# Optimization experiments

Hardware: AMD Instinct MI355X
Metric: run time of the kernel (lower is better)

## Reference

```python
import jax, jax.numpy as jnp
import numpy as np

TEMP_DIM = 36      # V
HIDDEN   = 128     # d
HEADS    = 4
STATIC   = 16
MAX_LEN  = 500
SEQ_T    = 256
BATCH    = 32


def _xavier(k, shape):
    lim = np.sqrt(6.0 / (shape[0] + shape[1]))
    return jax.random.uniform(k, shape, jnp.float32, -lim, lim)


def setup_inputs() -> dict:
    d, V, S, T, B = HIDDEN, TEMP_DIM, STATIC, SEQ_T, BATCH
    key = jax.random.key(0)
    ks = jax.random.split(key, 16)
    return dict(
        Xtemp=jax.random.normal(ks[0], (T, B, V), jnp.float32),
        Xtimes=jax.random.uniform(ks[1], (T, B, 1), jnp.float32) * MAX_LEN,
        Xstatic=jax.random.normal(ks[2], (B, S), jnp.float32),
        mask=jax.random.randint(ks[3], (T, B, V), 0, 2, jnp.int32),
        # MultiHeadAttention params
        Wq=_xavier(ks[4], (d, d)), Wk=_xavier(ks[5], (d, d)), Wv=_xavier(ks[6], (d, d)),
        # grouped Conv1d(V, V*d, 1, groups=V): per-variable scale+bias -> (V,d)
        temp_w=jax.random.normal(ks[7], (V, d), jnp.float32) * 0.5,
        temp_b=jnp.zeros((V, d), jnp.float32),
        # static embedding Linear(S, V*d)
        emb_W=_xavier(ks[8], (S, V * d)), emb_b=jnp.zeros((V * d,), jnp.float32),
        # MLP: Conv1d(V*d,4d,1)+BN+GELU, Conv1d(4d,d,1)+BN+GELU
        mlp_W1=_xavier(ks[9], (4 * d, V * d)), mlp_b1=jnp.zeros((4 * d,), jnp.float32),
        bn1_g=jnp.ones((4 * d,), jnp.float32), bn1_b=jnp.zeros((4 * d,), jnp.float32),
        mlp_W2=_xavier(ks[10], (d, 4 * d)), mlp_b2=jnp.zeros((d,), jnp.float32),
        bn2_g=jnp.ones((d,), jnp.float32), bn2_b=jnp.zeros((d,), jnp.float32),
        ln_g=jnp.ones((d,), jnp.float32), ln_b=jnp.zeros((d,), jnp.float32),
    )


def _batchnorm(x, g, b):
    # train-mode BatchNorm1d over (B, T) for x:(B, C, T), biased variance, eps=1e-5
    mu = x.mean((0, 2), keepdims=True)
    var = x.var((0, 2), keepdims=True)
    return (x - mu) * jax.lax.rsqrt(var + 1e-5) * g[None, :, None] + b[None, :, None]


def reference(Xtemp, Xtimes, Xstatic, mask, Wq, Wk, Wv, temp_w, temp_b,
              emb_W, emb_b, mlp_W1, mlp_b1, bn1_g, bn1_b,
              mlp_W2, mlp_b2, bn2_g, bn2_b, ln_g, ln_b):
    T, B, V = Xtemp.shape
    d = Wq.shape[0]
    h = HEADS
    dk = d // h

    xt = Xtemp.transpose(1, 2, 0)                      # (B,V,T)
    m = mask.astype(jnp.float32).transpose(1, 2, 0)    # (B,V,T)

    # grouped 1x1 conv == per-variable affine lift to d channels
    Htemp = xt[:, :, None, :] * temp_w[None, :, :, None] + temp_b[None, :, :, None]  # (B,V,d,T)
    Htemp = Htemp.transpose(0, 2, 1, 3)                # (B,d,V,T)

    # positional encoding
    timescales = jnp.power(jnp.float32(MAX_LEN), jnp.linspace(0.0, 1.0, d // 2))
    scaled = Xtimes / timescales                       # (T,B,d//2)
    pe = jnp.concatenate([jnp.sin(scaled), jnp.cos(scaled)], axis=-1)  # (T,B,d)
    Hpos = pe.transpose(1, 2, 0)[:, :, None, :]        # (B,d,1,T)

    emb = (Xstatic @ emb_W + emb_b).reshape(B, V, d).transpose(0, 2, 1)[..., None]  # (B,d,V,1)
    H = Htemp + Hpos + emb                             # (B,d,V,T)

    # masked temporal mean per variable
    mk = m[:, None]                                    # (B,1,V,T)
    h2 = (H * mk).sum(-1)                              # (B,d,V)
    lt = mk.sum(-1) + 1.0                              # (B,1,V)
    h4 = (h2 / lt).transpose(0, 2, 1)                  # (B,V,d)

    # multi-head variable-vs-variable scores
    scale = 1.0 / np.sqrt(dk).astype(np.float32)
    q = (h4 @ Wq).reshape(B, V, h, dk) * scale
    k = (h4 @ Wk).reshape(B, V, h, dk) * scale
    A = jnp.einsum('bvhd,buhd->bhvu', q, k)            # (B,h,V,V)
    mean_v = h4 @ Wv                                   # (B,V,d)

    # per-timestep key masking, broadcast softmax over last (key-variable) dim
    key_mask = m.transpose(0, 2, 1)                    # (B,T,V)
    A4 = A[:, :, None, :, :] - 1e6 * (1.0 - key_mask[:, None, :, None, :])  # (B,h,T,V,V)
    S = jax.nn.softmax(A4, axis=-1)                    # (B,h,T,V,V)

    H2 = H.reshape(B, h, dk, V, T)
    v2 = jnp.einsum('bhtvu,bhdut->bhdvt', S, H2)       # (B,h,dk,V,T)
    v3 = v2.reshape(B, d, V, T)
    v4 = v3 + mean_v.transpose(0, 2, 1)[:, :, :, None]
    v5 = v4.reshape(B, d * V, T)

    y1 = jnp.einsum('bct,oc->bot', v5, mlp_W1) + mlp_b1[None, :, None]
    y1 = jax.nn.gelu(_batchnorm(y1, bn1_g, bn1_b), approximate=False)
    y2 = jnp.einsum('bct,oc->bot', y1, mlp_W2) + mlp_b2[None, :, None]
    z = jax.nn.gelu(_batchnorm(y2, bn2_g, bn2_b), approximate=False)   # (B,d,T)

    # residual LayerNorm over channel dim
    zt = z.transpose(0, 2, 1)                          # (B,T,d)
    mu = zt.mean(-1, keepdims=True)
    var = zt.var(-1, keepdims=True)
    zn = (zt - mu) * jax.lax.rsqrt(var + 1e-5) * ln_g + ln_b
    return z + zn.transpose(0, 2, 1)                   # (B,d,T)
```

## Files before the change

### kernel.cpp

```cpp
#include <hip/hip_runtime.h>
#include <hip/hip_bf16.h>
#include <math.h>

#define T_  256
#define B_  32
#define V_  36
#define D_  128
#define H_  4
#define DK_ 32
#define S_  16
#define D4_ 512
#define K1_ 4608
#define M_  8192

typedef __hip_bfloat16 bf16;
typedef __attribute__((ext_vector_type(8))) short short8;
typedef __attribute__((ext_vector_type(4))) float f32x4;

__device__ __forceinline__ float gelu_f(float x){
    return 0.5f * x * (1.0f + erff(x * 0.70710678118654752f));
}

__device__ __forceinline__ unsigned short bf16_bits(float x){
    bf16 h = __float2bfloat16(x);
    return *reinterpret_cast<unsigned short*>(&h);
}

#define GLD16(g, l) __builtin_amdgcn_global_load_lds( \
    (const __attribute__((address_space(1))) void*)(g), \
    (__attribute__((address_space(3))) void*)(l), 16, 0, 0)

__global__ void k_pe(const float* __restrict__ Xtimes, float* __restrict__ PE){
    int bt = blockIdx.x;
    int b = bt >> 8, t = bt & 255;
    int dd = threadIdx.x;
    float x = Xtimes[t*B_ + b];
    int i = (dd < 64) ? dd : dd - 64;
    float sc = x * exp2f(-(float)i * (8.965784284662087f / 63.0f));
    PE[(size_t)bt*D_ + dd] = (dd < 64) ? sinf(sc) : cosf(sc);
}

__global__ void k_cb(const float* __restrict__ Xstatic, const float* __restrict__ embW,
                     const float* __restrict__ embB, const float* __restrict__ tempB,
                     float* __restrict__ CB){
    int bv = blockIdx.x;
    int b = bv / V_, v = bv - (bv / V_) * V_;
    int dd = threadIdx.x;
    int c = v*D_ + dd;
    float acc = tempB[c] + embB[c];
    #pragma unroll
    for(int s = 0; s < S_; ++s) acc = fmaf(Xstatic[b*S_+s], embW[s*K1_ + c], acc);
    CB[(size_t)bv*D_ + dd] = acc;
}

__global__ void k_h4(const float* __restrict__ Xtemp, const int* __restrict__ mask,
                     const float* __restrict__ PE, const float* __restrict__ tempW,
                     const float* __restrict__ CB, float* __restrict__ H4){
    __shared__ float s_m[T_];
    __shared__ float s_r0[256];
    __shared__ float s_r1[256];
    __shared__ float s_p[2][D_];
    int bv = blockIdx.x;
    int b = bv / V_, v = bv - (bv / V_) * V_;
    int tid = threadIdx.x;
    float mval = (float)mask[(tid*B_ + b)*V_ + v];
    float xval = Xtemp[(tid*B_ + b)*V_ + v];
    s_m[tid]  = mval;
    s_r0[tid] = mval;
    s_r1[tid] = mval * xval;
    __syncthreads();
    for(int off = 128; off > 0; off >>= 1){
        if(tid < off){ s_r0[tid] += s_r0[tid+off]; s_r1[tid] += s_r1[tid+off]; }
        __syncthreads();
    }
    float sm = s_r0[0], sx = s_r1[0];
    int dd = tid & 127, half = tid >> 7;
    float sp = 0.f;
    for(int tt = half*128; tt < half*128 + 128; ++tt)
        sp = fmaf(s_m[tt], PE[(size_t)(b*T_ + tt)*D_ + dd], sp);
    s_p[half][dd] = sp;
    __syncthreads();
    if(tid < D_){
        float spv = s_p[0][tid] + s_p[1][tid];
        float h2 = fmaf(sx, tempW[v*D_ + tid], fmaf(sm, CB[(size_t)bv*D_ + tid], spv));
        H4[(size_t)bv*D_ + tid] = h2 / (sm + 1.0f);
    }
}

__global__ void k_qkv(const float* __restrict__ H4, const float* __restrict__ Wq,
                      const float* __restrict__ Wk, const float* __restrict__ Wv,
                      float* __restrict__ QS, float* __restrict__ KS, float* __restrict__ MV){
    __shared__ float s_h[D_];
    int bv = blockIdx.x;
    int o = threadIdx.x;
    s_h[o] = H4[(size_t)bv*D_ + o];
    __syncthreads();
    float aq = 0.f, ak = 0.f, av = 0.f;
    #pragma unroll 8
    for(int kk = 0; kk < D_; ++kk){
        float hv = s_h[kk];
        aq = fmaf(hv, Wq[kk*D_ + o], aq);
        ak = fmaf(hv, Wk[kk*D_ + o], ak);
        av = fmaf(hv, Wv[kk*D_ + o], av);
    }
    const float scale = 0.17677669529663687f;
    QS[(size_t)bv*D_ + o] = aq * scale;
    KS[(size_t)bv*D_ + o] = ak * scale;
    MV[(size_t)bv*D_ + o] = av;
}

__global__ void k_attE(const float* __restrict__ QS, const float* __restrict__ KS,
                       float* __restrict__ E){
    int id = blockIdx.x;
    int v  = id % V_;
    int bh = id / V_;
    int hh = bh & 3, b = bh >> 2;
    int u = threadIdx.x;
    __shared__ float s_q[DK_];
    if(u < DK_) s_q[u] = QS[(size_t)(b*V_ + v)*D_ + hh*DK_ + u];
    __syncthreads();
    float a = -INFINITY;
    if(u < V_){
        a = 0.f;
        const float* kp = &KS[(size_t)(b*V_ + u)*D_ + hh*DK_];
        #pragma unroll
        for(int kk = 0; kk < DK_; ++kk) a = fmaf(s_q[kk], kp[kk], a);
    }
    float m = a;
    for(int off = 32; off > 0; off >>= 1) m = fmaxf(m, __shfl_xor(m, off));
    if(u < V_) E[(size_t)id*V_ + u] = expf(a - m);
}

__global__ __launch_bounds__(256,2) void k_v5(const int* __restrict__ mask,
        const float* __restrict__ Xtemp, const float* __restrict__ tempW,
        const float* __restrict__ CB, const float* __restrict__ E,
        const float* __restrict__ MV, const float* __restrict__ PE,
        bf16* __restrict__ V5){
    __shared__ __align__(16) float s_tw2[9*D_*4];
    __shared__ __align__(16) float s_cb2[9*D_*4];
    __shared__ __align__(16) float s_em2[9*144*4];
    __shared__ float s_rden[144];
    __shared__ __align__(16) float s_xt[V_];
    __shared__ float s_mk[V_];
    int bt = blockIdx.x;
    int b = bt >> 8, t = bt & 255;
    int tid = threadIdx.x;
    if(tid < V_){
        s_xt[tid] = Xtemp[(t*B_ + b)*V_ + tid];
        s_mk[tid] = (float)mask[(t*B_ + b)*V_ + tid];
    }
    for(int i = tid; i < V_*D_; i += 256){
        int u = i >> 7, dd = i & 127;
        int idx = ((u >> 2)*D_ + dd)*4 + (u & 3);
        s_tw2[idx] = tempW[i];
        s_cb2[idx] = CB[(size_t)b*K1_ + i];
    }
    __syncthreads();
    for(int i = tid; i < 144*V_; i += 256){
        int hv = i / V_, u = i - hv*V_;
        s_em2[((u >> 2)*144 + hv)*4 + (u & 3)] = E[(size_t)b*144*V_ + i] * s_mk[u];
    }
    __syncthreads();
    if(tid < 144){
        float den = 0.f;
        #pragma unroll
        for(int u = 0; u < V_; ++u) den += s_em2[((u>>2)*144 + tid)*4 + (u&3)];
        if(den == 0.0f){
            den = 0.f;
            #pragma unroll
            for(int u = 0; u < V_; ++u){
                float e = E[(size_t)b*144*V_ + tid*V_ + u];
                s_em2[((u>>2)*144 + tid)*4 + (u&3)] = e;
                den += e;
            }
        }
        s_rden[tid] = 1.0f / den;
    }
    __syncthreads();

    int dd = tid & 127, half = tid >> 7;
    int hh = dd >> 5;
    int vbase = half * 18;
    int hvb = hh*V_ + vbase;
    float acc[18] = {};
    #pragma unroll
    for(int u4 = 0; u4 < 9; ++u4){
        float4 xt4 = *(const float4*)&s_xt[u4*4];
        float4 tw4 = *(const float4*)&s_tw2[(u4*D_ + dd)*4];
        float4 cb4 = *(const float4*)&s_cb2[(u4*D_ + dd)*4];
        float4 w4;
        w4.x = fmaf(xt4.x, tw4.x, cb4.x);
        w4.y = fmaf(xt4.y, tw4.y, cb4.y);
        w4.z = fmaf(xt4.z, tw4.z, cb4.z);
        w4.w = fmaf(xt4.w, tw4.w, cb4.w);
        #pragma unroll
        for(int v = 0; v < 18; ++v){
            float4 e4 = *(const float4*)&s_em2[(u4*144 + hvb + v)*4];
            acc[v] = fmaf(e4.x, w4.x, fmaf(e4.y, w4.y,
                     fmaf(e4.z, w4.z, fmaf(e4.w, w4.w, acc[v]))));
        }
    }
    float pe = PE[(size_t)bt*D_ + dd];
    size_t obase = (size_t)bt*K1_ + dd*V_ + vbase;
    unsigned int* o32 = (unsigned int*)&V5[obase];
    #pragma unroll
    for(int v = 0; v < 18; v += 2){
        float r0 = fmaf(acc[v],   s_rden[hvb + v],
                        MV[((size_t)b*V_ + vbase + v)*D_ + dd] + pe);
        float r1 = fmaf(acc[v+1], s_rden[hvb + v + 1],
                        MV[((size_t)b*V_ + vbase + v + 1)*D_ + dd] + pe);
        o32[v >> 1] = (unsigned int)bf16_bits(r0) |
                      ((unsigned int)bf16_bits(r1) << 16);
    }
}

__global__ void k_cast(const float* __restrict__ src, bf16* __restrict__ dst){
    int i = (blockIdx.x*256 + threadIdx.x)*4;
    float4 v = *(const float4*)&src[i];
    dst[i+0] = __float2bfloat16(v.x);
    dst[i+1] = __float2bfloat16(v.y);
    dst[i+2] = __float2bfloat16(v.z);
    dst[i+3] = __float2bfloat16(v.w);
}

__global__ __launch_bounds__(256) void k_gemm1(const bf16* __restrict__ A,
        const bf16* __restrict__ Bw, const float* __restrict__ bias,
        float* __restrict__ C){
    __shared__ __align__(16) bf16 As[128*32];
    __shared__ __align__(16) bf16 Bs[64*32];
    int bid = blockIdx.x;
    int L = (bid & 7)*64 + (bid >> 3);
    int nb = L & 7, mb = L >> 3;
    int m0 = mb * 128, n0 = nb * 64;
    int tid = threadIdx.x;
    int w = tid >> 6, l = tid & 63;
    int wr = w >> 1, wc = w & 1;
    int r = l & 15, kg = l >> 4;
    f32x4 acc[4][2] = {};

    int ua0 = w*64 + l;
    int ua1 = (4+w)*64 + l;
    const bf16* ga0 = A  + (size_t)(m0 + (ua0 >> 2))*K1_ + (ua0 & 3)*8;
    const bf16* ga1 = A  + (size_t)(m0 + (ua1 >> 2))*K1_ + (ua1 & 3)*8;
    const bf16* gb  = Bw + (size_t)(n0 + (ua0 >> 2))*K1_ + (ua0 & 3)*8;
    bf16* la0 = &As[(size_t)w*512];
    bf16* la1 = &As[(size_t)(4+w)*512];
    bf16* lb  = &Bs[(size_t)w*512];

    for(int k0 = 0; k0 < K1_; k0 += 32){
        GLD16(ga0 + k0, la0);
        GLD16(ga1 + k0, la1);
        GLD16(gb  + k0, lb);
        __syncthreads();
        short8 af[4], bfr[2];
        #pragma unroll
        for(int m = 0; m < 4; ++m)
            af[m] = *(const short8*)&As[(wr*64 + m*16 + r)*32 + kg*8];
        #pragma unroll
        for(int n = 0; n < 2; ++n)
            bfr[n] = *(const short8*)&Bs[(wc*32 + n*16 + r)*32 + kg*8];
        #pragma unroll
        for(int m = 0; m < 4; ++m)
            #pragma unroll
            for(int n = 0; n < 2; ++n)
                acc[m][n] = __builtin_amdgcn_mfma_f32_16x16x32_bf16(
                                af[m], bfr[n], acc[m][n], 0, 0, 0);
        __syncthreads();
    }
    #pragma unroll
    for(int m = 0; m < 4; ++m){
        int rowb = m0 + wr*64 + m*16 + kg*4;
        #pragma unroll
        for(int n = 0; n < 2; ++n){
            int col = n0 + wc*32 + n*16 + r;
            float bv = bias[col];
            #pragma unroll
            for(int i = 0; i < 4; ++i)
                C[(size_t)(rowb + i)*D4_ + col] = acc[m][n][i] + bv;
        }
    }
}

__global__ void k_stats(const float* __restrict__ X, int C, float* __restrict__ ST){
    int r0 = blockIdx.x * 64;
    int tid = threadIdx.x;
    for(int c = tid; c < C; c += 256){
        float s = 0.f, q = 0.f;
        for(int r = 0; r < 64; ++r){
            float v = X[(size_t)(r0 + r)*C + c];
            s += v;
            q = fmaf(v, v, q);
        }
        atomicAdd(&ST[c], s);
        atomicAdd(&ST[C + c], q);
    }
}

__global__ void k_bnfin(const float* __restrict__ ST, const float* __restrict__ g,
                        const float* __restrict__ bb, int C, float* __restrict__ P){
    int c = blockIdx.x * blockDim.x + threadIdx.x;
    if(c < C){
        float mu  = ST[c] * (1.0f / M_);
        float var = ST[C + c] * (1.0f / M_) - mu*mu;
        float sc  = g[c] * rsqrtf(var + 1e-5f);
        P[c]     = sc;
        P[C + c] = bb[c] - mu*sc;
    }
}

__global__ __launch_bounds__(256) void k_gemm2(const float* __restrict__ Y1,
        const float* __restrict__ P1, const float* __restrict__ W2,
        const float* __restrict__ b2, float* __restrict__ Z){
    __shared__ __align__(16) float As[16][68];
    __shared__ __align__(16) float Bs[16][68];
    int tid = threadIdx.x;
    int m0 = blockIdx.x * 64, n0 = blockIdx.y * 64;
    float acc[4][4] = {};
    int arow = tid >> 2, ac = (tid & 3) * 4;
    int ty = tid >> 4, tx = tid & 15;
    for(int k0 = 0; k0 < D4_; k0 += 16){
        float4 a = *(const float4*)&Y1[(size_t)(m0 + arow)*D4_ + k0 + ac];
        float4 w = *(const float4*)&W2[(size_t)(n0 + arow)*D4_ + k0 + ac];
        As[ac+0][arow] = gelu_f(fmaf(a.x, P1[k0+ac+0], P1[D4_ + k0+ac+0]));
        As[ac+1][arow] = gelu_f(fmaf(a.y, P1[k0+ac+1], P1[D4_ + k0+ac+1]));
        As[ac+2][arow] = gelu_f(fmaf(a.z, P1[k0+ac+2], P1[D4_ + k0+ac+2]));
        As[ac+3][arow] = gelu_f(fmaf(a.w, P1[k0+ac+3], P1[D4_ + k0+ac+3]));
        Bs[ac+0][arow] = w.x; Bs[ac+1][arow] = w.y;
        Bs[ac+2][arow] = w.z; Bs[ac+3][arow] = w.w;
        __syncthreads();
        #pragma unroll
        for(int kk = 0; kk < 16; ++kk){
            float4 x = *(const float4*)&As[kk][ty*4];
            float4 y = *(const float4*)&Bs[kk][tx*4];
            float av[4] = {x.x,x.y,x.z,x.w};
            float bv[4] = {y.x,y.y,y.z,y.w};
            #pragma unroll
            for(int i = 0; i < 4; ++i)
                #pragma unroll
                for(int j = 0; j < 4; ++j)
                    acc[i][j] = fmaf(av[i], bv[j], acc[i][j]);
        }
        __syncthreads();
    }
    #pragma unroll
    for(int i = 0; i < 4; ++i){
        int row = m0 + ty*4 + i, col = n0 + tx*4;
        float4 o;
        o.x = acc[i][0] + b2[col+0];
        o.y = acc[i][1] + b2[col+1];
        o.z = acc[i][2] + b2[col+2];
        o.w = acc[i][3] + b2[col+3];
        *(float4*)&Z[(size_t)row*D_ + col] = o;
    }
}

__global__ __launch_bounds__(256) void k_final(const float* __restrict__ Z,
        const float* __restrict__ P2, const float* __restrict__ lng,
        const float* __restrict__ lnb, float* __restrict__ out){
    __shared__ float s_z[64*129];
    __shared__ float s_mu[64];
    __shared__ float s_rs[64];
    int b  = blockIdx.x >> 2;
    int t0 = (blockIdx.x & 3) * 64;
    int tid = threadIdx.x;
    #pragma unroll
    for(int i = 0; i < 32; ++i){
        int idx = tid + i*256;
        int row = idx >> 7, col = idx & 127;
        float v = Z[(size_t)(b*T_ + t0 + row)*D_ + col];
        s_z[row*129 + col] = gelu_f(fmaf(v, P2[col], P2[D_ + col]));
    }
    __syncthreads();
    if(tid < 64){
        float s = 0.f;
        #pragma unroll
        for(int j = 0; j < D_; ++j) s += s_z[tid*129 + j];
        float mu = s * (1.0f / D_);
        float q = 0.f;
        #pragma unroll
        for(int j = 0; j < D_; ++j){
            float dv = s_z[tid*129 + j] - mu;
            q = fmaf(dv, dv, q);
        }
        s_mu[tid] = mu;
        s_rs[tid] = rsqrtf(q * (1.0f / D_) + 1e-5f);
    }
    __syncthreads();
    int o  = tid & 127;
    int th = tid >> 7;
    float g  = lng[o];
    float be = lnb[o];
    #pragma unroll
    for(int j4 = 0; j4 < 8; ++j4){
        float4 ov;
        #pragma unroll
        for(int q = 0; q < 4; ++q){
            int tt = th*32 + j4*4 + q;
            float z = s_z[tt*129 + o];
            float zn = fmaf((z - s_mu[tt]) * s_rs[tt], g, be);
            (&ov.x)[q] = z + zn;
        }
        *(float4*)&out[((size_t)(b*D_ + o))*T_ + t0 + th*32 + j4*4] = ov;
    }
}

extern "C" void kernel_launch(void* const* d_in, const int* in_sizes, int n_in,
                              void* d_out, int out_size, void* d_ws, size_t ws_size,
                              hipStream_t stream){
    const float* Xtemp   = (const float*)d_in[0];
    const float* Xtimes  = (const float*)d_in[1];
    const float* Xstatic = (const float*)d_in[2];
    const int*   mask    = (const int*)  d_in[3];
    const float* Wq      = (const float*)d_in[4];
    const float* Wk      = (const float*)d_in[5];
    const float* Wv      = (const float*)d_in[6];
    const float* tempW   = (const float*)d_in[7];
    const float* tempB   = (const float*)d_in[8];
    const float* embW    = (const float*)d_in[9];
    const float* embB    = (const float*)d_in[10];
    const float* W1      = (const float*)d_in[11];
    const float* b1      = (const float*)d_in[12];
    const float* bn1g    = (const float*)d_in[13];
    const float* bn1b    = (const float*)d_in[14];
    const float* W2      = (const float*)d_in[15];
    const float* b2      = (const float*)d_in[16];
    const float* bn2g    = (const float*)d_in[17];
    const float* bn2b    = (const float*)d_in[18];
    const float* lng     = (const float*)d_in[19];
    const float* lnb     = (const float*)d_in[20];
    float* out = (float*)d_out;

    float* w = (float*)d_ws;
    float* PE = w;  w += (size_t)M_ * D_;
    float* CB = w;  w += (size_t)B_ * V_ * D_;
    float* H4 = w;  w += (size_t)B_ * V_ * D_;
    float* QS = w;  w += (size_t)B_ * V_ * D_;
    float* KS = w;  w += (size_t)B_ * V_ * D_;
    float* MV = w;  w += (size_t)B_ * V_ * D_;
    float* E  = w;  w += (size_t)B_ * H_ * V_ * V_;
    float* Y1 = w;  w += (size_t)M_ * D4_;
    float* Z1 = w;  w += (size_t)M_ * D_;
    float* ST1 = w; w += 1024;
    float* ST2 = w; w += 256;
    float* P1  = w; w += 1024;
    float* P2  = w; w += 256;
    bf16* V5  = (bf16*)w;
    bf16* W1b = (bf16*)(w + ((size_t)M_ * K1_) / 2);

    hipMemsetAsync(ST1, 0, (1024 + 256) * sizeof(float), stream);

    k_pe  <<<M_, D_, 0, stream>>>(Xtimes, PE);
    k_cb  <<<B_*V_, D_, 0, stream>>>(Xstatic, embW, embB, tempB, CB);
    k_cast<<<(D4_*K1_)/1024, 256, 0, stream>>>(W1, W1b);
    k_h4  <<<B_*V_, 256, 0, stream>>>(Xtemp, mask, PE, tempW, CB, H4);
    k_qkv <<<B_*V_, D_, 0, stream>>>(H4, Wq, Wk, Wv, QS, KS, MV);
    k_attE<<<B_*H_*V_, 64, 0, stream>>>(QS, KS, E);
    k_v5  <<<M_, 256, 0, stream>>>(mask, Xtemp, tempW, CB, E, MV, PE, V5);
    k_gemm1<<<512, 256, 0, stream>>>(V5, W1b, b1, Y1);
    k_stats<<<M_/64, 256, 0, stream>>>(Y1, D4_, ST1);
    k_bnfin<<<2, 256, 0, stream>>>(ST1, bn1g, bn1b, D4_, P1);
    k_gemm2<<<dim3(M_/64, D_/64), 256, 0, stream>>>(Y1, P1, W2, b2, Z1);
    k_stats<<<M_/64, 256, 0, stream>>>(Z1, D_, ST2);
    k_bnfin<<<1, 128, 0, stream>>>(ST2, bn2g, bn2b, D_, P2);
    k_final<<<B_*(T_/64), 256, 0, stream>>>(Z1, P2, lng, lnb, out);
}
```

Measured before the change: 456.0 us.

## Restructure attention-value kernel, widen GEMM1 K-tile with swizzle, halve stats rows

k_pe now precomputes per-timestep mask and value factors (QQ) with the all-masked fallback already folded in. The new k_v5 handles two timesteps per block, takes pre-packed tempW/CB layouts from global memory, and accumulates the softmax denominator inside the main loop instead of in a separate shared-memory pass. GEMM1 moves to a 64-wide K tile with XOR-swizzled LDS addressing to cut bank conflicts and halve the number of loop iterations and barriers. k_stats uses 32 rows per block to launch more blocks. The costs are extra packing kernels and scalar bf16 stores in k_v5, and the fallback now treats fully-masked timesteps as all-ones, which may not match the previous path exactly.

```diff
diff --git a/kernel.cpp b/kernel.cpp
--- a/kernel.cpp
+++ b/kernel.cpp
@@ -21,28 +21,45 @@
     return 0.5f * x * (1.0f + erff(x * 0.70710678118654752f));
 }
 
-__device__ __forceinline__ unsigned short bf16_bits(float x){
-    bf16 h = __float2bfloat16(x);
-    return *reinterpret_cast<unsigned short*>(&h);
+__device__ __forceinline__ float dot4(float4 a, float4 b){
+    return fmaf(a.x, b.x, fmaf(a.y, b.y, fmaf(a.z, b.z, a.w * b.w)));
 }
 
 #define GLD16(g, l) __builtin_amdgcn_global_load_lds( \
     (const __attribute__((address_space(1))) void*)(g), \
     (__attribute__((address_space(3))) void*)(l), 16, 0, 0)
 
-__global__ void k_pe(const float* __restrict__ Xtimes, float* __restrict__ PE){
+__global__ void k_pe(const float* __restrict__ Xtimes, const float* __restrict__ Xtemp,
+                     const int* __restrict__ mask, float* __restrict__ PE,
+                     float* __restrict__ QQ){
     int bt = blockIdx.x;
     int b = bt >> 8, t = bt & 255;
-    int dd = threadIdx.x;
+    int tid = threadIdx.x;
     float x = Xtimes[t*B_ + b];
-    int i = (dd < 64) ? dd : dd - 64;
+    int i = (tid < 64) ? tid : tid - 64;
     float sc = x * exp2f(-(float)i * (8.965784284662087f / 63.0f));
-    PE[(size_t)bt*D_ + dd] = (dd < 64) ? sinf(sc) : cosf(sc);
+    PE[(size_t)bt*D_ + tid] = (tid < 64) ? sinf(sc) : cosf(sc);
+    if(tid < 64){
+        float m = 0.f, xv = 0.f;
+        if(tid < V_){
+            m  = (float)mask[(t*B_ + b)*V_ + tid];
+            xv = Xtemp[(t*B_ + b)*V_ + tid];
+        }
+        float s = m;
+        #pragma unroll
+        for(int off = 32; off > 0; off >>= 1) s += __shfl_xor(s, off);
+        if(tid < V_){
+            float q0 = (s > 0.f) ? m : 1.f;
+            float q1 = (s > 0.f) ? m*xv : xv;
+            QQ[(size_t)bt*80 + tid]      = q1;
+            QQ[(size_t)bt*80 + 40 + tid] = q0;
+        }
+    }
 }
 
 __global__ void k_cb(const float* __restrict__ Xstatic, const float* __restrict__ embW,
                      const float* __restrict__ embB, const float* __restrict__ tempB,
-                     float* __restrict__ CB){
+                     float* __restrict__ CB, float* __restrict__ cbP){
     int bv = blockIdx.x;
     int b = bv / V_, v = bv - (bv / V_) * V_;
     int dd = threadIdx.x;
@@ -51,6 +68,12 @@
     #pragma unroll
     for(int s = 0; s < S_; ++s) acc = fmaf(Xstatic[b*S_+s], embW[s*K1_ + c], acc);
     CB[(size_t)bv*D_ + dd] = acc;
+    cbP[(((size_t)b*9 + (v >> 2))*D_ + dd)*4 + (v & 3)] = acc;
+}
+
+__global__ void k_packtw(const float* __restrict__ tempW, float* __restrict__ twP){
+    int v = blockIdx.x, dd = threadIdx.x;
+    twP[(((v >> 2))*D_ + dd)*4 + (v & 3)] = tempW[v*D_ + dd];
 }
 
 __global__ void k_h4(const float* __restrict__ Xtemp, const int* __restrict__ mask,
@@ -128,89 +151,83 @@
     }
     float m = a;
     for(int off = 32; off > 0; off >>= 1) m = fmaxf(m, __shfl_xor(m, off));
-    if(u < V_) E[(size_t)id*V_ + u] = expf(a - m);
-}
-
-__global__ __launch_bounds__(256,2) void k_v5(const int* __restrict__ mask,
-        const float* __restrict__ Xtemp, const float* __restrict__ tempW,
-        const float* __restrict__ CB, const float* __restrict__ E,
-        const float* __restrict__ MV, const float* __restrict__ PE,
-        bf16* __restrict__ V5){
-    __shared__ __align__(16) float s_tw2[9*D_*4];
-    __shared__ __align__(16) float s_cb2[9*D_*4];
-    __shared__ __align__(16) float s_em2[9*144*4];
-    __shared__ float s_rden[144];
-    __shared__ __align__(16) float s_xt[V_];
-    __shared__ float s_mk[V_];
-    int bt = blockIdx.x;
-    int b = bt >> 8, t = bt & 255;
-    int tid = threadIdx.x;
-    if(tid < V_){
-        s_xt[tid] = Xtemp[(t*B_ + b)*V_ + tid];
-        s_mk[tid] = (float)mask[(t*B_ + b)*V_ + tid];
-    }
-    for(int i = tid; i < V_*D_; i += 256){
-        int u = i >> 7, dd = i & 127;
-        int idx = ((u >> 2)*D_ + dd)*4 + (u & 3);
-        s_tw2[idx] = tempW[i];
-        s_cb2[idx] = CB[(size_t)b*K1_ + i];
-    }
-    __syncthreads();
-    for(int i = tid; i < 144*V_; i += 256){
-        int hv = i / V_, u = i - hv*V_;
-        s_em2[((u >> 2)*144 + hv)*4 + (u & 3)] = E[(size_t)b*144*V_ + i] * s_mk[u];
-    }
-    __syncthreads();
-    if(tid < 144){
-        float den = 0.f;
-        #pragma unroll
-        for(int u = 0; u < V_; ++u) den += s_em2[((u>>2)*144 + tid)*4 + (u&3)];
-        if(den == 0.0f){
-            den = 0.f;
-            #pragma unroll
-            for(int u = 0; u < V_; ++u){
-                float e = E[(size_t)b*144*V_ + tid*V_ + u];
-                s_em2[((u>>2)*144 + tid)*4 + (u&3)] = e;
-                den += e;
-            }
-        }
-        s_rden[tid] = 1.0f / den;
-    }
-    __syncthreads();
-
-    int dd = tid & 127, half = tid >> 7;
-    int hh = dd >> 5;
-    int vbase = half * 18;
-    int hvb = hh*V_ + vbase;
-    float acc[18] = {};
+    if(u < V_) E[(size_t)id*40 + u] = expf(a - m);
+}
+
+__global__ __launch_bounds__(256) void k_v5(const float* __restrict__ QQ,
+        const float* __restrict__ Eg, const float* __restrict__ twP,
+        const float* __restrict__ cbP, const float* __restrict__ MV,
+        const float* __restrict__ PE, bf16* __restrict__ V5){
+    __shared__ float s_E[4*1300];
+    int blk = blockIdx.x;
+    int b = blk >> 7, tp = blk & 127;
+    int bt0 = b*T_ + tp*2;
+    int tid = threadIdx.x;
+    int vq = tid >> 6, hh = (tid >> 4) & 3, j = tid & 15;
+    int dd0 = hh*32 + j, dd1 = dd0 + 16;
+
+    for(int i = tid; i < 144*9; i += 256){
+        int hv = i / 9, u4 = i - hv*9;
+        int hq = hv / 36, vr = hv - hq*36;
+        float4 e = *(const float4*)&Eg[((size_t)b*144 + hv)*40 + u4*4];
+        *(float4*)&s_E[hq*1300 + (u4*36 + vr)*4] = e;
+    }
+    __syncthreads();
+
+    float acc[2][2][9] = {};
+    float den[2][9]    = {};
     #pragma unroll
     for(int u4 = 0; u4 < 9; ++u4){
-        float4 xt4 = *(const float4*)&s_xt[u4*4];
-        float4 tw4 = *(const float4*)&s_tw2[(u4*D_ + dd)*4];
-        float4 cb4 = *(const float4*)&s_cb2[(u4*D_ + dd)*4];
-        float4 w4;
-        w4.x = fmaf(xt4.x, tw4.x, cb4.x);
-        w4.y = fmaf(xt4.y, tw4.y, cb4.y);
-        w4.z = fmaf(xt4.z, tw4.z, cb4.z);
-        w4.w = fmaf(xt4.w, tw4.w, cb4.w);
-        #pragma unroll
-        for(int v = 0; v < 18; ++v){
-            float4 e4 = *(const float4*)&s_em2[(u4*144 + hvb + v)*4];
-            acc[v] = fmaf(e4.x, w4.x, fmaf(e4.y, w4.y,
-                     fmaf(e4.z, w4.z, fmaf(e4.w, w4.w, acc[v]))));
-        }
-    }
-    float pe = PE[(size_t)bt*D_ + dd];
-    size_t obase = (size_t)bt*K1_ + dd*V_ + vbase;
-    unsigned int* o32 = (unsigned int*)&V5[obase];
-    #pragma unroll
-    for(int v = 0; v < 18; v += 2){
-        float r0 = fmaf(acc[v],   s_rden[hvb + v],
-                        MV[((size_t)b*V_ + vbase + v)*D_ + dd] + pe);
-        float r1 = fmaf(acc[v+1], s_rden[hvb + v + 1],
-                        MV[((size_t)b*V_ + vbase + v + 1)*D_ + dd] + pe);
-        o32[v >> 1] = (unsigned int)bf16_bits(r0) |
-                      ((unsigned int)bf16_bits(r1) << 16);
+        float4 q1a = *(const float4*)&QQ[(size_t)bt0*80 + u4*4];
+        float4 q0a = *(const float4*)&QQ[(size_t)bt0*80 + 40 + u4*4];
+        float4 q1b = *(const float4*)&QQ[(size_t)(bt0+1)*80 + u4*4];
+        float4 q0b = *(const float4*)&QQ[(size_t)(bt0+1)*80 + 40 + u4*4];
+        float4 tw0 = *(const float4*)&twP[(u4*D_ + dd0)*4];
+        float4 tw1 = *(const float4*)&twP[(u4*D_ + dd1)*4];
+        float4 cb0 = *(const float4*)&cbP[(((size_t)b*9 + u4)*D_ + dd0)*4];
+        float4 cb1 = *(const float4*)&cbP[(((size_t)b*9 + u4)*D_ + dd1)*4];
+        float4 w00, w01, w10, w11;
+        w00.x = fmaf(q1a.x, tw0.x, q0a.x*cb0.x); w00.y = fmaf(q1a.y, tw0.y, q0a.y*cb0.y);
+        w00.z = fmaf(q1a.z, tw0.z, q0a.z*cb0.z); w00.w = fmaf(q1a.w, tw0.w, q0a.w*cb0.w);
+        w01.x = fmaf(q1a.x, tw1.x, q0a.x*cb1.x); w01.y = fmaf(q1a.y, tw1.y, q0a.y*cb1.y);
+        w01.z = fmaf(q1a.z, tw1.z, q0a.z*cb1.z); w01.w = fmaf(q1a.w, tw1.w, q0a.w*cb1.w);
+        w10.x = fmaf(q1b.x, tw0.x, q0b.x*cb0.x); w10.y = fmaf(q1b.y, tw0.y, q0b.y*cb0.y);
+        w10.z = fmaf(q1b.z, tw0.z, q0b.z*cb0.z); w10.w = fmaf(q1b.w, tw0.w, q0b.w*cb0.w);
+        w11.x = fmaf(q1b.x, tw1.x, q0b.x*cb1.x); w11.y = fmaf(q1b.y, tw1.y, q0b.y*cb1.y);
+        w11.z = fmaf(q1b.z, tw1.z, q0b.z*cb1.z); w11.w = fmaf(q1b.w, tw1.w, q0b.w*cb1.w);
+        int ebase = hh*1300 + (u4*36 + vq*9)*4;
+        #pragma unroll
+        for(int vv = 0; vv < 9; ++vv){
+            float4 e = *(const float4*)&s_E[ebase + vv*4];
+            den[0][vv] += dot4(e, q0a);
+            den[1][vv] += dot4(e, q0b);
+            acc[0][0][vv] += dot4(e, w00);
+            acc[0][1][vv] += dot4(e, w01);
+            acc[1][0][vv] += dot4(e, w10);
+            acc[1][1][vv] += dot4(e, w11);
+        }
+    }
+    float mv[2][9];
+    #pragma unroll
+    for(int vv = 0; vv < 9; ++vv){
+        mv[0][vv] = MV[((size_t)b*V_ + vq*9 + vv)*D_ + dd0];
+        mv[1][vv] = MV[((size_t)b*V_ + vq*9 + vv)*D_ + dd1];
+    }
+    #pragma unroll
+    for(int t = 0; t < 2; ++t){
+        size_t bt = bt0 + t;
+        float rd[9];
+        #pragma unroll
+        for(int vv = 0; vv < 9; ++vv) rd[vv] = 1.0f / den[t][vv];
+        float pe0 = PE[bt*D_ + dd0];
+        float pe1 = PE[bt*D_ + dd1];
+        bf16* op0 = V5 + bt*K1_ + dd0*V_ + vq*9;
+        bf16* op1 = V5 + bt*K1_ + dd1*V_ + vq*9;
+        #pragma unroll
+        for(int vv = 0; vv < 9; ++vv){
+            op0[vv] = __float2bfloat16(fmaf(acc[t][0][vv], rd[vv], mv[0][vv] + pe0));
+            op1[vv] = __float2bfloat16(fmaf(acc[t][1][vv], rd[vv], mv[1][vv] + pe1));
+        }
     }
 }
 
@@ -226,8 +243,8 @@
 __global__ __launch_bounds__(256) void k_gemm1(const bf16* __restrict__ A,
         const bf16* __restrict__ Bw, const float* __restrict__ bias,
         float* __restrict__ C){
-    __shared__ __align__(16) bf16 As[128*32];
-    __shared__ __align__(16) bf16 Bs[64*32];
+    __shared__ __align__(16) bf16 As[128*64];
+    __shared__ __align__(16) bf16 Bs[64*64];
     int bid = blockIdx.x;
     int L = (bid & 7)*64 + (bid >> 3);
     int nb = L & 7, mb = L >> 3;
@@ -238,33 +255,57 @@
     int r = l & 15, kg = l >> 4;
     f32x4 acc[4][2] = {};
 
-    int ua0 = w*64 + l;
-    int ua1 = (4+w)*64 + l;
-    const bf16* ga0 = A  + (size_t)(m0 + (ua0 >> 2))*K1_ + (ua0 & 3)*8;
-    const bf16* ga1 = A  + (size_t)(m0 + (ua1 >> 2))*K1_ + (ua1 & 3)*8;
-    const bf16* gb  = Bw + (size_t)(n0 + (ua0 >> 2))*K1_ + (ua0 & 3)*8;
-    bf16* la0 = &As[(size_t)w*512];
-    bf16* la1 = &As[(size_t)(4+w)*512];
-    bf16* lb  = &Bs[(size_t)w*512];
-
-    for(int k0 = 0; k0 < K1_; k0 += 32){
-        GLD16(ga0 + k0, la0);
-        GLD16(ga1 + k0, la1);
-        GLD16(gb  + k0, lb);
+    int sA0 = 0*256 + w*64 + l;
+    int sA1 = 1*256 + w*64 + l;
+    int sA2 = 2*256 + w*64 + l;
+    int sA3 = 3*256 + w*64 + l;
+    int sB0 = 0*256 + w*64 + l;
+    int sB1 = 1*256 + w*64 + l;
+    const bf16* gA0 = A + (size_t)(m0 + (sA0>>3))*K1_ + ((sA0&7) ^ ((sA0>>3)&7))*8;
+    const bf16* gA1 = A + (size_t)(m0 + (sA1>>3))*K1_ + ((sA1&7) ^ ((sA1>>3)&7))*8;
+    const bf16* gA2 = A + (size_t)(m0 + (sA2>>3))*K1_ + ((sA2&7) ^ ((sA2>>3)&7))*8;
+    const bf16* gA3 = A + (size_t)(m0 + (sA3>>3))*K1_ + ((sA3&7) ^ ((sA3>>3)&7))*8;
+    const bf16* gB0 = Bw + (size_t)(n0 + (sB0>>3))*K1_ + ((sB0&7) ^ ((sB0>>3)&7))*8;
+    const bf16* gB1 = Bw + (size_t)(n0 + (sB1>>3))*K1_ + ((sB1&7) ^ ((sB1>>3)&7))*8;
+    bf16* lA0 = &As[(0*256 + w*64)*8];
+    bf16* lA1 = &As[(1*256 + w*64)*8];
+    bf16* lA2 = &As[(2*256 + w*64)*8];
+    bf16* lA3 = &As[(3*256 + w*64)*8];
+    bf16* lB0 = &Bs[(0*256 + w*64)*8];
+    bf16* lB1 = &Bs[(1*256 + w*64)*8];
+
+    for(int k0 = 0; k0 < K1_; k0 += 64){
+        GLD16(gA0 + k0, lA0);
+        GLD16(gA1 + k0, lA1);
+        GLD16(gA2 + k0, lA2);
+        GLD16(gA3 + k0, lA3);
+        GLD16(gB0 + k0, lB0);
+        GLD16(gB1 + k0, lB1);
         __syncthreads();
-        short8 af[4], bfr[2];
-        #pragma unroll
-        for(int m = 0; m < 4; ++m)
-            af[m] = *(const short8*)&As[(wr*64 + m*16 + r)*32 + kg*8];
-        #pragma unroll
-        for(int n = 0; n < 2; ++n)
-            bfr[n] = *(const short8*)&Bs[(wc*32 + n*16 + r)*32 + kg*8];
-        #pragma unroll
-        for(int m = 0; m < 4; ++m)
+        short8 af[2][4], bfr[2][2];
+        #pragma unroll
+        for(int kh = 0; kh < 2; ++kh){
             #pragma unroll
-            for(int n = 0; n < 2; ++n)
-                acc[m][n] = __builtin_amdgcn_mfma_f32_16x16x32_bf16(
-                                af[m], bfr[n], acc[m][n], 0, 0, 0);
+            for(int m = 0; m < 4; ++m){
+                int row = wr*64 + m*16 + r;
+                int e = (row*64 + kh*32 + kg*8) ^ ((r & 7) << 3);
+                af[kh][m] = *(const short8*)&As[e];
+            }
+            #pragma unroll
+            for(int n = 0; n < 2; ++n){
+                int row = wc*32 + n*16 + r;
+                int e = (row*64 + kh*32 + kg*8) ^ ((r & 7) << 3);
+                bfr[kh][n] = *(const short8*)&Bs[e];
+            }
+        }
+        #pragma unroll
+        for(int kh = 0; kh < 2; ++kh)
+            #pragma unroll
+            for(int m = 0; m < 4; ++m)
+                #pragma unroll
+                for(int n = 0; n < 2; ++n)
+                    acc[m][n] = __builtin_amdgcn_mfma_f32_16x16x32_bf16(
+                                    af[kh][m], bfr[kh][n], acc[m][n], 0, 0, 0);
         __syncthreads();
     }
     #pragma unroll
@@ -282,11 +323,11 @@
 }
 
 __global__ void k_stats(const float* __restrict__ X, int C, float* __restrict__ ST){
-    int r0 = blockIdx.x * 64;
+    int r0 = blockIdx.x * 32;
     int tid = threadIdx.x;
     for(int c = tid; c < C; c += 256){
         float s = 0.f, q = 0.f;
-        for(int r = 0; r < 64; ++r){
+        for(int r = 0; r < 32; ++r){
             float v = X[(size_t)(r0 + r)*C + c];
             s += v;
             q = fmaf(v, v, q);
@@ -433,11 +474,14 @@
     float* w = (float*)d_ws;
     float* PE = w;  w += (size_t)M_ * D_;
     float* CB = w;  w += (size_t)B_ * V_ * D_;
+    float* cbP= w;  w += (size_t)B_ * 9 * D_ * 4;
+    float* twP= w;  w += (size_t)9 * D_ * 4;
     float* H4 = w;  w += (size_t)B_ * V_ * D_;
     float* QS = w;  w += (size_t)B_ * V_ * D_;
     float* KS = w;  w += (size_t)B_ * V_ * D_;
     float* MV = w;  w += (size_t)B_ * V_ * D_;
-    float* E  = w;  w += (size_t)B_ * H_ * V_ * V_;
+    float* E  = w;  w += (size_t)B_ * 144 * 40;
+    float* QQ = w;  w += (size_t)M_ * 80;
     float* Y1 = w;  w += (size_t)M_ * D4_;
     float* Z1 = w;  w += (size_t)M_ * D_;
     float* ST1 = w; w += 1024;
@@ -449,18 +493,19 @@
 
     hipMemsetAsync(ST1, 0, (1024 + 256) * sizeof(float), stream);
 
-    k_pe  <<<M_, D_, 0, stream>>>(Xtimes, PE);
-    k_cb  <<<B_*V_, D_, 0, stream>>>(Xstatic, embW, embB, tempB, CB);
-    k_cast<<<(D4_*K1_)/1024, 256, 0, stream>>>(W1, W1b);
-    k_h4  <<<B_*V_, 256, 0, stream>>>(Xtemp, mask, PE, tempW, CB, H4);
-    k_qkv <<<B_*V_, D_, 0, stream>>>(H4, Wq, Wk, Wv, QS, KS, MV);
-    k_attE<<<B_*H_*V_, 64, 0, stream>>>(QS, KS, E);
-    k_v5  <<<M_, 256, 0, stream>>>(mask, Xtemp, tempW, CB, E, MV, PE, V5);
-    k_gemm1<<<512, 256, 0, stream>>>(V5, W1b, b1, Y1);
-    k_stats<<<M_/64, 256, 0, stream>>>(Y1, D4_, ST1);
-    k_bnfin<<<2, 256, 0, stream>>>(ST1, bn1g, bn1b, D4_, P1);
-    k_gemm2<<<dim3(M_/64, D_/64), 256, 0, stream>>>(Y1, P1, W2, b2, Z1);
-    k_stats<<<M_/64, 256, 0, stream>>>(Z1, D_, ST2);
-    k_bnfin<<<1, 128, 0, stream>>>(ST2, bn2g, bn2b, D_, P2);
-    k_final<<<B_*(T_/64), 256, 0, stream>>>(Z1, P2, lng, lnb, out);
-}
+    k_pe    <<<M_, D_, 0, stream>>>(Xtimes, Xtemp, mask, PE, QQ);
+    k_cb    <<<B_*V_, D_, 0, stream>>>(Xstatic, embW, embB, tempB, CB, cbP);
+    k_packtw<<<V_, D_, 0, stream>>>(tempW, twP);
+    k_cast  <<<(D4_*K1_)/1024, 256, 0, stream>>>(W1, W1b);
+    k_h4    <<<B_*V_, 256, 0, stream>>>(Xtemp, mask, PE, tempW, CB, H4);
+    k_qkv   <<<B_*V_, D_, 0, stream>>>(H4, Wq, Wk, Wv, QS, KS, MV);
+    k_attE  <<<B_*H_*V_, 64, 0, stream>>>(QS, KS, E);
+    k_v5    <<<B_*(T_/2), 256, 0, stream>>>(QQ, E, twP, cbP, MV, PE, V5);
+    k_gemm1 <<<512, 256, 0, stream>>>(V5, W1b, b1, Y1);
+    k_stats <<<M_/32, 256, 0, stream>>>(Y1, D4_, ST1);
+    k_bnfin <<<2, 256, 0, stream>>>(ST1, bn1g, bn1b, D4_, P1);
+    k_gemm2 <<<dim3(M_/64, D_/64), 256, 0, stream>>>(Y1, P1, W2, b2, Z1);
+    k_stats <<<M_/32, 256, 0, stream>>>(Z1, D_, ST2);
+    k_bnfin <<<1, 128, 0, stream>>>(ST2, bn2g, bn2b, D_, P2);
+    k_final <<<B_*(T_/64), 256, 0, stream>>>(Z1, P2, lng, lnb, out);
+}
```

New measurement: 776.0 us. 1.7x slower.
